# Performance work log

Measured on AMD Instinct MI355X. Metric: run time of the kernel, lower is better.

## Reference

```python
import jax, jax.numpy as jnp
import numpy as np

T, B, DIM, N = 2048, 16, 1024, 64
INIT_BETA_BIAS = 2.0
EPS = 1e-6


def setup_inputs() -> dict:
    key = jax.random.key(0)
    ks = jax.random.split(key, 6)
    xavier = np.sqrt(2.0 / (N + DIM)).astype(np.float32)
    return {
        "x": jax.random.normal(ks[0], (T, B, DIM), dtype=jnp.float32),
        "S0": jnp.zeros((B, N, N), dtype=jnp.float32),
        "W_k": jax.random.normal(ks[1], (N, DIM), dtype=jnp.float32) * xavier,
        "W_v": jax.random.normal(ks[2], (N, DIM), dtype=jnp.float32) * xavier,
        "W_q": jax.random.normal(ks[3], (N, DIM), dtype=jnp.float32) * xavier,
        "W_beta": jax.random.normal(ks[4], (N, DIM), dtype=jnp.float32) * xavier,
        "b_beta": jnp.full((N,), INIT_BETA_BIAS, dtype=jnp.float32),
    }


def reference(x, S0, W_k, W_v, W_q, W_beta, b_beta):
    # Batched projections: [T, B, dim] @ [dim, n] -> [T, B, n]
    k_all = jnp.einsum("tbd,nd->tbn", x, W_k)
    v_all = jnp.einsum("tbd,nd->tbn", x, W_v)
    q_all = jnp.einsum("tbd,nd->tbn", x, W_q)
    g_all = jax.nn.sigmoid(jnp.einsum("tbd,nd->tbn", x, W_beta) + b_beta)

    def step(S, inp):
        k, v, q, g = inp  # each [B, n]
        k_norm = k / (jnp.linalg.norm(k, axis=-1, keepdims=True) + EPS)
        retrieved = jnp.einsum("bij,bj->bi", S, k_norm)
        delta = v - retrieved
        S_new = g[:, :, None] * S + delta[:, :, None] * k_norm[:, None, :]
        Sq = jnp.einsum("bij,bj->bi", S_new, q)
        out = Sq * jax.nn.silu(Sq)  # self-gated output
        return S_new, out

    S_final, output = jax.lax.scan(step, S0, (k_all, v_all, q_all, g_all))
    return output, S_final
```

## Files before the change

kernel.cpp:

```cpp
#include <hip/hip_runtime.h>
#include <math.h>

#define T_STEPS 2048
#define BATCH   16
#define DIM     1024
#define NSTATE  64
#define NFIELD  256
#define PROJ_TSTRIDE (BATCH * NFIELD)
static constexpr float EPS = 1e-6f;

#define AS1 __attribute__((address_space(1)))
#define AS3 __attribute__((address_space(3)))

typedef _Float16 f16x8 __attribute__((ext_vector_type(8)));
typedef _Float16 f16x4 __attribute__((ext_vector_type(4)));
typedef float    f32x4 __attribute__((ext_vector_type(4)));

template <int CTRL>
__device__ __forceinline__ float dpp_pmul(float x) {
    int yi = __builtin_amdgcn_update_dpp(0x3f800000, __float_as_int(x),
                                         CTRL, 0xF, 0xF, false);
    return x * __int_as_float(yi);
}
template <int CTRL>
__device__ __forceinline__ float dpp_add(float x) {
    int yi = __builtin_amdgcn_update_dpp(0, __float_as_int(x), CTRL, 0xF, 0xF, true);
    return x + __int_as_float(yi);
}


#define PBM   128
#define KSTEP 64
#define NKS   (DIM / KSTEP)

__global__ __launch_bounds__(256) void prep_w16(
    const float* __restrict__ Wk, const float* __restrict__ Wv,
    const float* __restrict__ Wq, const float* __restrict__ Wb,
    _Float16* __restrict__ W16)
{
    const int flat = blockIdx.x * 256 + threadIdx.x;
    const int lane = flat & 63;
    const int st   = (flat >> 6) & 31;
    const int ks   = flat >> 11;
    const int cg = st & 15, kc2 = st >> 4;
    const int col = cg * 16 + (lane & 15);
    const int field = col >> 6, wrow = col & 63;
    const float* Wf = (field == 0 ? Wk : field == 1 ? Wv : field == 2 ? Wq : Wb);
    const float* src = Wf + (size_t)wrow * DIM + ks * 64 + kc2 * 32 + (lane >> 4) * 8;
    const float4 a = *(const float4*)(src);
    const float4 b = *(const float4*)(src + 4);
    f16x8 r;
    r[0] = (_Float16)a.x; r[1] = (_Float16)a.y; r[2] = (_Float16)a.z; r[3] = (_Float16)a.w;
    r[4] = (_Float16)b.x; r[5] = (_Float16)b.y; r[6] = (_Float16)b.z; r[7] = (_Float16)b.w;
    *(f16x8*)(W16 + (size_t)flat * 8) = r;
}

__global__ __launch_bounds__(512, 1) void proj_mfma(
    const float* __restrict__ x, const _Float16* __restrict__ W16,
    const float* __restrict__ bb, float* __restrict__ proj)
{
    __shared__ _Float16 Asub[2][16][64][8];
    __shared__ _Float16 Bsub[2][32][64][8];

    const int tid = threadIdx.x;
    const int w = tid >> 6, wl = tid & 63;
    const int wm = w >> 2, wn = w & 3;
    const int l15 = wl & 15, lr = wl >> 4;
    const size_t mbase = (size_t)blockIdx.x * PBM;

    _Float16* const abase = &Asub[0][0][0][0];
    _Float16* const bbase = &Bsub[0][0][0][0];

    const float* asrc[4];
    int aoff[4];
    #pragma unroll
    for (int it = 0; it < 4; ++it) {
        const int fid = it * 512 + tid;
        const int row = fid >> 4, kq = (fid & 15) * 4;
        asrc[it] = x + (mbase + row) * (size_t)DIM + kq;
        aoff[it] = ((kq >> 5) * 8 + (row >> 4)) * 512
                 + ((row & 15) + ((kq >> 3) & 3) * 16) * 8
                 + (kq & 7);
    }
    const _Float16* bsrc[4];
    int boff[4];
    #pragma unroll
    for (int m = 0; m < 4; ++m) {
        const int st = w * 4 + m;
        bsrc[m] = W16 + ((size_t)st * 64 + wl) * 8;
        boff[m] = st * 512;
    }

    auto stageB = [&](int ks, int buf) {
        #pragma unroll
        for (int m = 0; m < 4; ++m) {
            const _Float16* g = bsrc[m] + (size_t)ks * 16384;
            void* lp = (char*)bbase + (size_t)(buf * 16384 + boff[m]) * 2;
            __builtin_amdgcn_global_load_lds((const AS1 void*)g, (AS3 void*)lp, 16, 0, 0);
        }
    };

    float4 h0[4], h1[4];
    auto loadA = [&](int ks, float4* h) {
        #pragma unroll
        for (int it = 0; it < 4; ++it)
            h[it] = *(const float4*)(asrc[it] + ks * KSTEP);
    };
    auto writeA = [&](const float4* h, int buf) {
        #pragma unroll
        for (int it = 0; it < 4; ++it) {
            f16x4 v;
            v[0] = (_Float16)h[it].x; v[1] = (_Float16)h[it].y;
            v[2] = (_Float16)h[it].z; v[3] = (_Float16)h[it].w;
            *(f16x4*)(abase + buf * 8192 + aoff[it]) = v;
        }
    };

    f32x4 acc[4][4] = {};

    loadA(0, h0);
    stageB(0, 0);
    loadA(1, h1);
    writeA(h0, 0);
    __syncthreads();

    #pragma unroll
    for (int ks = 0; ks < NKS; ++ks) {
        const int buf = ks & 1;
        if (ks + 1 < NKS) stageB(ks + 1, buf ^ 1);
        if (ks + 2 < NKS) loadA(ks + 2, (ks & 1) ? h1 : h0);

        #pragma unroll
        for (int kc = 0; kc < 2; ++kc) {
            f16x8 af[4], bf[4];
            #pragma unroll
            for (int mf = 0; mf < 4; ++mf)
                af[mf] = *(const f16x8*)&Asub[buf][kc * 8 + wm * 4 + mf][wl][0];
            #pragma unroll
            for (int nf = 0; nf < 4; ++nf)
                bf[nf] = *(const f16x8*)&Bsub[buf][kc * 16 + wn * 4 + nf][wl][0];
            #pragma unroll
            for (int mf = 0; mf < 4; ++mf)
                #pragma unroll
                for (int nf = 0; nf < 4; ++nf)
                    acc[mf][nf] = __builtin_amdgcn_mfma_f32_16x16x32_f16(
                        af[mf], bf[nf], acc[mf][nf], 0, 0, 0);
        }

        if (ks + 1 < NKS) writeA((ks & 1) ? h0 : h1, buf ^ 1);
        __syncthreads();
    }

    if (wn == 0) {
        #pragma unroll
        for (int mf = 0; mf < 4; ++mf) {
            f32x4 s = acc[mf][0] * acc[mf][0];
            #pragma unroll
            for (int nf = 1; nf < 4; ++nf) s += acc[mf][nf] * acc[mf][nf];
            #pragma unroll
            for (int r = 0; r < 4; ++r) {
                float t = s[r];
                t += __shfl_xor(t, 1); t += __shfl_xor(t, 2);
                t += __shfl_xor(t, 4); t += __shfl_xor(t, 8);
                const float sc = 1.f / (sqrtf(t) + EPS);
                #pragma unroll
                for (int nf = 0; nf < 4; ++nf) acc[mf][nf][r] *= sc;
            }
        }
    }
    if (wn == 3) {
        #pragma unroll
        for (int nf = 0; nf < 4; ++nf) {
            const float bv = bb[nf * 16 + l15];
            #pragma unroll
            for (int mf = 0; mf < 4; ++mf)
                #pragma unroll
                for (int r = 0; r < 4; ++r)
                    acc[mf][nf][r] = 1.f / (1.f + __expf(-(acc[mf][nf][r] + bv)));
        }
    }

    #pragma unroll
    for (int mf = 0; mf < 4; ++mf)
        #pragma unroll
        for (int r = 0; r < 4; ++r) {
            float* dst = proj + (mbase + wm * 64 + mf * 16 + lr * 4 + r) * NFIELD
                              + wn * 64 + l15;
            dst[0]  = acc[mf][0][r];
            dst[16] = acc[mf][1][r];
            dst[32] = acc[mf][2][r];
            dst[48] = acc[mf][3][r];
        }
}


#define CH 32
#define NCHUNK (T_STEPS / CH)

__global__ __launch_bounds__(256) void mn_prep(
    const float* __restrict__ proj, float* __restrict__ MN)
{
    __shared__ float K[32][68], Q[32][68];
    const int bch = blockIdx.x;
    const int b = bch >> 6, ch = bch & 63;
    const int tid = threadIdx.x;

    {
        const int t0 = tid >> 3, pp = tid & 7;
        const float* base = proj + ((size_t)(ch * 32 + t0) * BATCH + b) * NFIELD;
        *(float4*)&K[t0][8 * pp]     = *(const float4*)(base + 8 * pp);
        *(float4*)&K[t0][8 * pp + 4] = *(const float4*)(base + 8 * pp + 4);
        *(float4*)&Q[t0][8 * pp]     = *(const float4*)(base + 128 + 8 * pp);
        *(float4*)&Q[t0][8 * pp + 4] = *(const float4*)(base + 128 + 8 * pp + 4);
    }
    __syncthreads();

    const int t = tid & 31, ub = tid >> 5;
    float mm[4] = {0.f, 0.f, 0.f, 0.f}, nn[4] = {0.f, 0.f, 0.f, 0.f};
    #pragma unroll 4
    for (int db = 0; db < 16; ++db) {
        const float4 kt = *(const float4*)&K[t][4 * db];
        #pragma unroll
        for (int uu = 0; uu < 4; ++uu) {
            const float4 ku = *(const float4*)&K[ub * 4 + uu][4 * db];
            const float4 qu = *(const float4*)&Q[ub * 4 + uu][4 * db];
            mm[uu] = fmaf(kt.x, ku.x, fmaf(kt.y, ku.y,
                     fmaf(kt.z, ku.z, fmaf(kt.w, ku.w, mm[uu]))));
            nn[uu] = fmaf(kt.x, qu.x, fmaf(kt.y, qu.y,
                     fmaf(kt.z, qu.z, fmaf(kt.w, qu.w, nn[uu]))));
        }
    }
    float* dstb = MN + ((size_t)bch * 32) * 64;
    #pragma unroll
    for (int uu = 0; uu < 4; ++uu) {
        const int u = ub * 4 + uu;
        dstb[(size_t)u * 64 + t]      = (t < u)  ? mm[uu] : 0.f;
        dstb[(size_t)u * 64 + 32 + t] = (t <= u) ? nn[uu] : 0.f;
    }
}


__global__ __launch_bounds__(256, 1) void scan_kernel(
    const float* __restrict__ proj,
    const float* __restrict__ MN,
    const float* __restrict__ S0,
    float* __restrict__ out,
    float* __restrict__ Sfin)
{
    __shared__ float KQ[2][CH][128];
    __shared__ float VGT[2][16][CH];
    __shared__ float SROW[8][64];

    const int tid  = threadIdx.x;
    const int w    = tid >> 6, wl = tid & 63;
    const int half = wl >> 5, u = wl & 31;
    const int gid  = 2 * w + half;
    const int b    = blockIdx.x >> 3;
    const int i0   = (blockIdx.x & 7) * 8;
    const int i    = i0 + gid;

    {
        const float2 s2 = *(const float2*)(S0 + ((size_t)(b * 64 + i)) * 64 + 2 * u);
        *(float2*)&SROW[gid][2 * u] = s2;
    }

    const float* pb = proj + (size_t)b * NFIELD;

    const int l31 = wl & 31;
    const int glq = wl & 15;
    const int hlf = (l31 >= 16);
    auto stage = [&](int c2, int nb) {
        const float* cbase = pb + (size_t)c2 * CH * PROJ_TSTRIDE;
        #pragma unroll
        for (int m = 0; m < 4; ++m) {
            const int n = w * 4 + m;
            const int s = 2 * n + (wl >> 5);
            const int field = (hlf ? 128 : 0) + 4 * (glq ^ (s & 7));
            const float* g = cbase + (size_t)s * PROJ_TSTRIDE + field;
            void* lp = (char*)&KQ[nb][0][0] + n * 1024;
            __builtin_amdgcn_global_load_lds((const AS1 void*)g, (AS3 void*)lp, 16, 0, 0);
        }
        #pragma unroll
        for (int m = 0; m < 2; ++m) {
            const int p = w * 2 + m;
            const int f = 2 * p + (wl >> 5);
            const int col = wl & 31;
            const int field = (f < 8) ? (64 + i0 + f) : (192 + i0 + (f - 8));
            const float* g = cbase + (size_t)col * PROJ_TSTRIDE + field;
            void* lp = (char*)&VGT[nb][0][0] + p * 256;
            __builtin_amdgcn_global_load_lds((const AS1 void*)g, (AS3 void*)lp, 4, 0, 0);
        }
    };

    stage(0, 0);
    __syncthreads();

    for (int c = 0; c < NCHUNK; ++c) {
        const int cb = c & 1;
        if (c + 1 < NCHUNK) stage(c + 1, cb ^ 1);

        const float (*KQc)[128] = KQ[cb];
        const float (*VGTc)[CH] = VGT[cb];

        float Mreg[32], Nreg[32];
        {
            const float* mnb = MN + (((size_t)b * NCHUNK + c) * 32 + u) * 64;
            #pragma unroll
            for (int k = 0; k < 8; ++k) {
                const float4 t4 = *(const float4*)(mnb + 4 * k);
                Mreg[4 * k] = t4.x; Mreg[4 * k + 1] = t4.y;
                Mreg[4 * k + 2] = t4.z; Mreg[4 * k + 3] = t4.w;
            }
            #pragma unroll
            for (int k = 0; k < 8; ++k) {
                const float4 t4 = *(const float4*)(mnb + 32 + 4 * k);
                Nreg[4 * k] = t4.x; Nreg[4 * k + 1] = t4.y;
                Nreg[4 * k + 2] = t4.z; Nreg[4 * k + 3] = t4.w;
            }
        }

        const float v_u = VGTc[gid][u];
        const float g_u = VGTc[8 + gid][u];
        float P = g_u;
        P = dpp_pmul<0x111>(P);
        P = dpp_pmul<0x112>(P);
        P = dpp_pmul<0x114>(P);
        P = dpp_pmul<0x118>(P);
        {
            const int t15 = __builtin_amdgcn_ds_swizzle(__float_as_int(P), (15 << 5));
            const float pl = __int_as_float(t15);
            P = (u >= 16) ? P * pl : P;
        }
        const float Pm1  = P / g_u;
        const float invP = 1.0f / P;

        float acc = 0.f, accq = 0.f;
        #pragma unroll
        for (int a4 = 0; a4 < 16; ++a4) {
            const int L = 4 * (a4 ^ (u & 7));
            const float4 s4 = *(const float4*)&SROW[gid][4 * a4];
            const float4 k4 = *(const float4*)&KQc[u][L];
            const float4 q4 = *(const float4*)&KQc[u][64 + L];
            acc  = fmaf(s4.x, k4.x, fmaf(s4.y, k4.y,
                   fmaf(s4.z, k4.z, fmaf(s4.w, k4.w, acc))));
            accq = fmaf(s4.x, q4.x, fmaf(s4.y, q4.y,
                   fmaf(s4.z, q4.z, fmaf(s4.w, q4.w, accq))));
        }

        float2 supd = make_float2(0.f, 0.f);
#define SWEEP_STEP(T)                                                          \
        {                                                                      \
            const float e_ = (v_u - Pm1 * acc) * invP;                         \
            const int ei_ = __builtin_amdgcn_ds_swizzle(__float_as_int(e_),    \
                                                        ((T) << 5));           \
            const float eb_ = __int_as_float(ei_);                             \
            acc  = fmaf(eb_, Mreg[T], acc);                                    \
            accq = fmaf(eb_, Nreg[T], accq);                                   \
            const float2 kk_ = *(const float2*)&KQc[T][(2 * u) ^ (4 * ((T) & 7))]; \
            supd.x = fmaf(eb_, kk_.x, supd.x);                                 \
            supd.y = fmaf(eb_, kk_.y, supd.y);                                 \
        }
        SWEEP_STEP(0)  SWEEP_STEP(1)  SWEEP_STEP(2)  SWEEP_STEP(3)
        SWEEP_STEP(4)  SWEEP_STEP(5)  SWEEP_STEP(6)  SWEEP_STEP(7)
        SWEEP_STEP(8)  SWEEP_STEP(9)  SWEEP_STEP(10) SWEEP_STEP(11)
        SWEEP_STEP(12) SWEEP_STEP(13) SWEEP_STEP(14) SWEEP_STEP(15)
        SWEEP_STEP(16) SWEEP_STEP(17) SWEEP_STEP(18) SWEEP_STEP(19)
        SWEEP_STEP(20) SWEEP_STEP(21) SWEEP_STEP(22) SWEEP_STEP(23)
        SWEEP_STEP(24) SWEEP_STEP(25) SWEEP_STEP(26) SWEEP_STEP(27)
        SWEEP_STEP(28) SWEEP_STEP(29) SWEEP_STEP(30) SWEEP_STEP(31)
#undef SWEEP_STEP

        {
            const int p31 = __builtin_amdgcn_ds_swizzle(__float_as_int(P), (31 << 5));
            const float Pc = __int_as_float(p31);
            float2 sold = *(const float2*)&SROW[gid][2 * u];
            sold.x = Pc * (sold.x + supd.x);
            sold.y = Pc * (sold.y + supd.y);
            *(float2*)&SROW[gid][2 * u] = sold;
        }
        {
            const float oq = P * accq;
            const float y = oq * oq / (1.f + __expf(-oq));
            out[((size_t)(c * CH + u) * BATCH + b) * 64 + i] = y;
        }

        __syncthreads();
    }

    {
        const float2 sf = *(const float2*)&SROW[gid][2 * u];
        *(float2*)(Sfin + ((size_t)(b * 64 + i)) * 64 + 2 * u) = sf;
    }
}

extern "C" void kernel_launch(void* const* d_in, const int* in_sizes, int n_in,
                              void* d_out, int out_size, void* d_ws, size_t ws_size,
                              hipStream_t stream) {
    const float* x  = (const float*)d_in[0];
    const float* S0 = (const float*)d_in[1];
    const float* Wk = (const float*)d_in[2];
    const float* Wv = (const float*)d_in[3];
    const float* Wq = (const float*)d_in[4];
    const float* Wb = (const float*)d_in[5];
    const float* bb = (const float*)d_in[6];

    float* out  = (float*)d_out;
    float* Sfin = out + (size_t)T_STEPS * BATCH * NSTATE;

    float*    proj = (float*)d_ws;
    float*    MN   = proj + (size_t)T_STEPS * BATCH * NFIELD;
    _Float16* W16  = (_Float16*)(MN + (size_t)BATCH * NCHUNK * 32 * 64);

    prep_w16<<<128, 256, 0, stream>>>(Wk, Wv, Wq, Wb, W16);
    proj_mfma<<<(T_STEPS * BATCH) / PBM, 512, 0, stream>>>(x, W16, bb, proj);
    mn_prep<<<BATCH * NCHUNK, 256, 0, stream>>>(proj, MN);
    scan_kernel<<<(BATCH * NSTATE) / 8, 256, 0, stream>>>(proj, MN, S0, out, Sfin);
}
```

Baseline: 422.0 us.

## Widen scan chunks to 64 steps with full-wave rows and fp16 MN staging

Chunk length doubles from 32 to 64 so each wave handles one state row across all 64 lanes. The per-chunk M/N correction matrices move to fp16 and are staged into LDS via async global-to-LDS loads instead of per-thread register loads. The sweep broadcasts through readlane instead of ds_swizzle, and outputs are staged in LDS for coalesced stores. The goal is to halve the number of chunk iterations and barriers and to raise parallelism, with 256 blocks instead of 128. The costs are a longer serial sweep per chunk, fp16 precision loss in the correction terms, and possible readlane overhead.

Result: faster. 385.6 us (-8.6%).

```diff
diff --git a/kernel.cpp b/kernel.cpp
--- a/kernel.cpp
+++ b/kernel.cpp
@@ -14,18 +14,17 @@
 
 typedef _Float16 f16x8 __attribute__((ext_vector_type(8)));
 typedef _Float16 f16x4 __attribute__((ext_vector_type(4)));
+typedef _Float16 f16x2 __attribute__((ext_vector_type(2)));
 typedef float    f32x4 __attribute__((ext_vector_type(4)));
 
-template <int CTRL>
+template <int CTRL, int RMASK>
 __device__ __forceinline__ float dpp_pmul(float x) {
     int yi = __builtin_amdgcn_update_dpp(0x3f800000, __float_as_int(x),
-                                         CTRL, 0xF, 0xF, false);
+                                         CTRL, RMASK, 0xF, false);
     return x * __int_as_float(yi);
 }
-template <int CTRL>
-__device__ __forceinline__ float dpp_add(float x) {
-    int yi = __builtin_amdgcn_update_dpp(0, __float_as_int(x), CTRL, 0xF, 0xF, true);
-    return x + __int_as_float(yi);
+__device__ __forceinline__ float rdlane(float x, int l) {
+    return __int_as_float(__builtin_amdgcn_readlane(__float_as_int(x), l));
 }
 
 
@@ -194,100 +193,122 @@
 }
 
 
-#define CH 32
+#define CH 64
 #define NCHUNK (T_STEPS / CH)
 
 __global__ __launch_bounds__(256) void mn_prep(
-    const float* __restrict__ proj, float* __restrict__ MN)
+    const float* __restrict__ proj, _Float16* __restrict__ MNg)
 {
-    __shared__ float K[32][68], Q[32][68];
+    __shared__ float K[64][68], Q[64][68];
     const int bch = blockIdx.x;
-    const int b = bch >> 6, ch = bch & 63;
+    const int bb2 = bch >> 5, ch = bch & 31;
     const int tid = threadIdx.x;
 
-    {
-        const int t0 = tid >> 3, pp = tid & 7;
-        const float* base = proj + ((size_t)(ch * 32 + t0) * BATCH + b) * NFIELD;
-        *(float4*)&K[t0][8 * pp]     = *(const float4*)(base + 8 * pp);
-        *(float4*)&K[t0][8 * pp + 4] = *(const float4*)(base + 8 * pp + 4);
-        *(float4*)&Q[t0][8 * pp]     = *(const float4*)(base + 128 + 8 * pp);
-        *(float4*)&Q[t0][8 * pp + 4] = *(const float4*)(base + 128 + 8 * pp + 4);
+    #pragma unroll
+    for (int it = 0; it < 8; ++it) {
+        const int s = it * 256 + tid;
+        const int row = s >> 5, half = (s >> 4) & 1, idx = s & 15;
+        const float* src = proj + ((size_t)(ch * 64 + row) * BATCH + bb2) * NFIELD
+                         + (half ? 128 : 0) + idx * 4;
+        const float4 v4 = *(const float4*)src;
+        if (half == 0) *(float4*)&K[row][idx * 4] = v4;
+        else           *(float4*)&Q[row][idx * 4] = v4;
     }
     __syncthreads();
 
-    const int t = tid & 31, ub = tid >> 5;
-    float mm[4] = {0.f, 0.f, 0.f, 0.f}, nn[4] = {0.f, 0.f, 0.f, 0.f};
-    #pragma unroll 4
-    for (int db = 0; db < 16; ++db) {
-        const float4 kt = *(const float4*)&K[t][4 * db];
-        #pragma unroll
-        for (int uu = 0; uu < 4; ++uu) {
-            const float4 ku = *(const float4*)&K[ub * 4 + uu][4 * db];
-            const float4 qu = *(const float4*)&Q[ub * 4 + uu][4 * db];
-            mm[uu] = fmaf(kt.x, ku.x, fmaf(kt.y, ku.y,
-                     fmaf(kt.z, ku.z, fmaf(kt.w, ku.w, mm[uu]))));
-            nn[uu] = fmaf(kt.x, qu.x, fmaf(kt.y, qu.y,
-                     fmaf(kt.z, qu.z, fmaf(kt.w, qu.w, nn[uu]))));
-        }
-    }
-    float* dstb = MN + ((size_t)bch * 32) * 64;
-    #pragma unroll
-    for (int uu = 0; uu < 4; ++uu) {
-        const int u = ub * 4 + uu;
-        dstb[(size_t)u * 64 + t]      = (t < u)  ? mm[uu] : 0.f;
-        dstb[(size_t)u * 64 + 32 + t] = (t <= u) ? nn[uu] : 0.f;
+    const int t0 = (tid >> 4) * 4, u0 = (tid & 15) * 4;
+    float m4[4][4] = {}, n4[4][4] = {};
+    #pragma unroll
+    for (int j4 = 0; j4 < 16; ++j4) {
+        float4 kt[4], ku[4], qu[4];
+        #pragma unroll
+        for (int r = 0; r < 4; ++r) {
+            kt[r] = *(const float4*)&K[t0 + r][4 * j4];
+            ku[r] = *(const float4*)&K[u0 + r][4 * j4];
+            qu[r] = *(const float4*)&Q[u0 + r][4 * j4];
+        }
+        #pragma unroll
+        for (int a2 = 0; a2 < 4; ++a2)
+            #pragma unroll
+            for (int c2 = 0; c2 < 4; ++c2) {
+                m4[a2][c2] = fmaf(kt[a2].x, ku[c2].x, fmaf(kt[a2].y, ku[c2].y,
+                             fmaf(kt[a2].z, ku[c2].z, fmaf(kt[a2].w, ku[c2].w, m4[a2][c2]))));
+                n4[a2][c2] = fmaf(kt[a2].x, qu[c2].x, fmaf(kt[a2].y, qu[c2].y,
+                             fmaf(kt[a2].z, qu[c2].z, fmaf(kt[a2].w, qu[c2].w, n4[a2][c2]))));
+            }
+    }
+    _Float16* dst = MNg + (size_t)bch * 64 * 128;
+    #pragma unroll
+    for (int a2 = 0; a2 < 4; ++a2) {
+        const int t = t0 + a2;
+        #pragma unroll
+        for (int c2 = 0; c2 < 4; ++c2) {
+            const int uu = u0 + c2;
+            f16x2 val;
+            val[0] = (_Float16)((uu > t)  ? m4[a2][c2] : 0.f);
+            val[1] = (_Float16)((uu >= t) ? n4[a2][c2] : 0.f);
+            *(f16x2*)&dst[(size_t)t * 128 + 2 * uu] = val;
+        }
     }
 }
 
 
 __global__ __launch_bounds__(256, 1) void scan_kernel(
     const float* __restrict__ proj,
-    const float* __restrict__ MN,
+    const _Float16* __restrict__ MNg,
     const float* __restrict__ S0,
     float* __restrict__ out,
     float* __restrict__ Sfin)
 {
-    __shared__ float KQ[2][CH][128];
-    __shared__ float VGT[2][16][CH];
-    __shared__ float SROW[8][64];
-
-    const int tid  = threadIdx.x;
-    const int w    = tid >> 6, wl = tid & 63;
-    const int half = wl >> 5, u = wl & 31;
-    const int gid  = 2 * w + half;
-    const int b    = blockIdx.x >> 3;
-    const int i0   = (blockIdx.x & 7) * 8;
-    const int i    = i0 + gid;
-
-    {
-        const float2 s2 = *(const float2*)(S0 + ((size_t)(b * 64 + i)) * 64 + 2 * u);
-        *(float2*)&SROW[gid][2 * u] = s2;
-    }
+    __shared__ float    KQ[2][CH][128];
+    __shared__ _Float16 MNh[2][CH][128];
+    __shared__ float    VG[2][CH][8];
+    __shared__ float    OUTb[2][CH][4];
+    __shared__ float    SROW[4][64];
+
+    const int tid = threadIdx.x;
+    const int w = tid >> 6, u = tid & 63;
+    const int b  = blockIdx.x >> 4;
+    const int i0 = (blockIdx.x & 15) * 4;
+    const int i  = i0 + w;
+
+    float S = S0[((size_t)(b * 64 + i)) * 64 + u];
+    SROW[w][u] = S;
 
     const float* pb = proj + (size_t)b * NFIELD;
-
-    const int l31 = wl & 31;
-    const int glq = wl & 15;
-    const int hlf = (l31 >= 16);
-    auto stage = [&](int c2, int nb) {
-        const float* cbase = pb + (size_t)c2 * CH * PROJ_TSTRIDE;
+    const _Float16* mnb = MNg + (size_t)b * NCHUNK * CH * 128;
+
+    const int kq_dw = (u & 31) * 4;
+    const int kq_f  = (kq_dw < 64) ? kq_dw : kq_dw + 64;
+    const int kq_t  = u >> 5;
+    const int mn_t  = u >> 4;
+    const int mn_by = (u & 15) * 16;
+    const int vg_t  = u >> 3;
+    const int vg_fi = u & 7;
+    const int vg_f  = (vg_fi < 4) ? (64 + i0 + vg_fi) : (192 + i0 + vg_fi - 4);
+
+    auto stage = [&](int c, int nb) {
+        const float* cbase = pb + (size_t)c * CH * PROJ_TSTRIDE;
+        #pragma unroll
+        for (int m = 0; m < 8; ++m) {
+            const int n = w * 8 + m;
+            const float* g = cbase + (size_t)(2 * n + kq_t) * PROJ_TSTRIDE + kq_f;
+            void* lp = (char*)&KQ[nb][0][0] + n * 1024;
+            __builtin_amdgcn_global_load_lds((const AS1 void*)g, (AS3 void*)lp, 16, 0, 0);
+        }
+        const char* mnc = (const char*)(mnb + (size_t)c * CH * 128);
         #pragma unroll
         for (int m = 0; m < 4; ++m) {
             const int n = w * 4 + m;
-            const int s = 2 * n + (wl >> 5);
-            const int field = (hlf ? 128 : 0) + 4 * (glq ^ (s & 7));
-            const float* g = cbase + (size_t)s * PROJ_TSTRIDE + field;
-            void* lp = (char*)&KQ[nb][0][0] + n * 1024;
+            const char* g = mnc + (size_t)(4 * n + mn_t) * 256 + mn_by;
+            void* lp = (char*)&MNh[nb][0][0] + n * 1024;
             __builtin_amdgcn_global_load_lds((const AS1 void*)g, (AS3 void*)lp, 16, 0, 0);
         }
         #pragma unroll
         for (int m = 0; m < 2; ++m) {
             const int p = w * 2 + m;
-            const int f = 2 * p + (wl >> 5);
-            const int col = wl & 31;
-            const int field = (f < 8) ? (64 + i0 + f) : (192 + i0 + (f - 8));
-            const float* g = cbase + (size_t)col * PROJ_TSTRIDE + field;
-            void* lp = (char*)&VGT[nb][0][0] + p * 256;
+            const float* g = cbase + (size_t)(p * 8 + vg_t) * PROJ_TSTRIDE + vg_f;
+            void* lp = (char*)&VG[nb][0][0] + p * 256;
             __builtin_amdgcn_global_load_lds((const AS1 void*)g, (AS3 void*)lp, 4, 0, 0);
         }
     };
@@ -296,101 +317,62 @@
     __syncthreads();
 
     for (int c = 0; c < NCHUNK; ++c) {
-        const int cb = c & 1;
-        if (c + 1 < NCHUNK) stage(c + 1, cb ^ 1);
-
-        const float (*KQc)[128] = KQ[cb];
-        const float (*VGTc)[CH] = VGT[cb];
-
-        float Mreg[32], Nreg[32];
-        {
-            const float* mnb = MN + (((size_t)b * NCHUNK + c) * 32 + u) * 64;
-            #pragma unroll
-            for (int k = 0; k < 8; ++k) {
-                const float4 t4 = *(const float4*)(mnb + 4 * k);
-                Mreg[4 * k] = t4.x; Mreg[4 * k + 1] = t4.y;
-                Mreg[4 * k + 2] = t4.z; Mreg[4 * k + 3] = t4.w;
-            }
-            #pragma unroll
-            for (int k = 0; k < 8; ++k) {
-                const float4 t4 = *(const float4*)(mnb + 32 + 4 * k);
-                Nreg[4 * k] = t4.x; Nreg[4 * k + 1] = t4.y;
-                Nreg[4 * k + 2] = t4.z; Nreg[4 * k + 3] = t4.w;
-            }
-        }
-
-        const float v_u = VGTc[gid][u];
-        const float g_u = VGTc[8 + gid][u];
+        const int cb2 = c & 1;
+        if (c + 1 < NCHUNK) stage(c + 1, cb2 ^ 1);
+
+        const float v_u = VG[cb2][u][w];
+        const float g_u = VG[cb2][u][4 + w];
         float P = g_u;
-        P = dpp_pmul<0x111>(P);
-        P = dpp_pmul<0x112>(P);
-        P = dpp_pmul<0x114>(P);
-        P = dpp_pmul<0x118>(P);
-        {
-            const int t15 = __builtin_amdgcn_ds_swizzle(__float_as_int(P), (15 << 5));
-            const float pl = __int_as_float(t15);
-            P = (u >= 16) ? P * pl : P;
-        }
-        const float Pm1  = P / g_u;
-        const float invP = 1.0f / P;
+        P = dpp_pmul<0x111, 0xF>(P);
+        P = dpp_pmul<0x112, 0xF>(P);
+        P = dpp_pmul<0x114, 0xF>(P);
+        P = dpp_pmul<0x118, 0xF>(P);
+        P = dpp_pmul<0x142, 0xA>(P);
+        P = dpp_pmul<0x143, 0xC>(P);
+        const float invP = __builtin_amdgcn_rcpf(P);
+        const float c1 = v_u * invP;
+        const float c2 = __builtin_amdgcn_rcpf(g_u);
 
         float acc = 0.f, accq = 0.f;
         #pragma unroll
-        for (int a4 = 0; a4 < 16; ++a4) {
-            const int L = 4 * (a4 ^ (u & 7));
-            const float4 s4 = *(const float4*)&SROW[gid][4 * a4];
-            const float4 k4 = *(const float4*)&KQc[u][L];
-            const float4 q4 = *(const float4*)&KQc[u][64 + L];
+        for (int j4 = 0; j4 < 16; ++j4) {
+            const int Cg = 4 * (j4 ^ (u & 15));
+            const float4 s4 = *(const float4*)&SROW[w][Cg];
+            const float4 k4 = *(const float4*)&KQ[cb2][u][Cg];
+            const float4 q4 = *(const float4*)&KQ[cb2][u][64 + Cg];
             acc  = fmaf(s4.x, k4.x, fmaf(s4.y, k4.y,
                    fmaf(s4.z, k4.z, fmaf(s4.w, k4.w, acc))));
             accq = fmaf(s4.x, q4.x, fmaf(s4.y, q4.y,
                    fmaf(s4.z, q4.z, fmaf(s4.w, q4.w, accq))));
         }
 
-        float2 supd = make_float2(0.f, 0.f);
-#define SWEEP_STEP(T)                                                          \
-        {                                                                      \
-            const float e_ = (v_u - Pm1 * acc) * invP;                         \
-            const int ei_ = __builtin_amdgcn_ds_swizzle(__float_as_int(e_),    \
-                                                        ((T) << 5));           \
-            const float eb_ = __int_as_float(ei_);                             \
-            acc  = fmaf(eb_, Mreg[T], acc);                                    \
-            accq = fmaf(eb_, Nreg[T], accq);                                   \
-            const float2 kk_ = *(const float2*)&KQc[T][(2 * u) ^ (4 * ((T) & 7))]; \
-            supd.x = fmaf(eb_, kk_.x, supd.x);                                 \
-            supd.y = fmaf(eb_, kk_.y, supd.y);                                 \
-        }
-        SWEEP_STEP(0)  SWEEP_STEP(1)  SWEEP_STEP(2)  SWEEP_STEP(3)
-        SWEEP_STEP(4)  SWEEP_STEP(5)  SWEEP_STEP(6)  SWEEP_STEP(7)
-        SWEEP_STEP(8)  SWEEP_STEP(9)  SWEEP_STEP(10) SWEEP_STEP(11)
-        SWEEP_STEP(12) SWEEP_STEP(13) SWEEP_STEP(14) SWEEP_STEP(15)
-        SWEEP_STEP(16) SWEEP_STEP(17) SWEEP_STEP(18) SWEEP_STEP(19)
-        SWEEP_STEP(20) SWEEP_STEP(21) SWEEP_STEP(22) SWEEP_STEP(23)
-        SWEEP_STEP(24) SWEEP_STEP(25) SWEEP_STEP(26) SWEEP_STEP(27)
-        SWEEP_STEP(28) SWEEP_STEP(29) SWEEP_STEP(30) SWEEP_STEP(31)
-#undef SWEEP_STEP
+        float supd = 0.f;
+        #pragma unroll
+        for (int T = 0; T < CH; ++T) {
+            const float e  = fmaf(-c2, acc, c1);
+            const float se = rdlane(e, T);
+            const f16x2 mn = *(const f16x2*)&MNh[cb2][T][2 * u];
+            const float kT = KQ[cb2][T][u];
+            acc  = fmaf(se, (float)mn[0], acc);
+            accq = fmaf(se, (float)mn[1], accq);
+            supd = fmaf(se, kT, supd);
+        }
+
+        const float Pc = rdlane(P, 63);
+        S = Pc * (S + supd);
+        SROW[w][u] = S;
+        const float oq = P * accq;
+        OUTb[cb2][u][w] = oq * oq / (1.f + __expf(-oq));
+
+        __syncthreads();
 
         {
-            const int p31 = __builtin_amdgcn_ds_swizzle(__float_as_int(P), (31 << 5));
-            const float Pc = __int_as_float(p31);
-            float2 sold = *(const float2*)&SROW[gid][2 * u];
-            sold.x = Pc * (sold.x + supd.x);
-            sold.y = Pc * (sold.y + supd.y);
-            *(float2*)&SROW[gid][2 * u] = sold;
-        }
-        {
-            const float oq = P * accq;
-            const float y = oq * oq / (1.f + __expf(-oq));
-            out[((size_t)(c * CH + u) * BATCH + b) * 64 + i] = y;
-        }
-
-        __syncthreads();
-    }
-
-    {
-        const float2 sf = *(const float2*)&SROW[gid][2 * u];
-        *(float2*)(Sfin + ((size_t)(b * 64 + i)) * 64 + 2 * u) = sf;
-    }
+            const int t = tid >> 2, col = tid & 3;
+            out[((size_t)(c * CH + t) * BATCH + b) * 64 + i0 + col] = OUTb[cb2][t][col];
+        }
+    }
+
+    Sfin[((size_t)(b * 64 + i)) * 64 + u] = S;
 }
 
 extern "C" void kernel_launch(void* const* d_in, const int* in_sizes, int n_in,
@@ -408,11 +390,11 @@
     float* Sfin = out + (size_t)T_STEPS * BATCH * NSTATE;
 
     float*    proj = (float*)d_ws;
-    float*    MN   = proj + (size_t)T_STEPS * BATCH * NFIELD;
-    _Float16* W16  = (_Float16*)(MN + (size_t)BATCH * NCHUNK * 32 * 64);
+    _Float16* MNg  = (_Float16*)(proj + (size_t)T_STEPS * BATCH * NFIELD);
+    _Float16* W16  = MNg + (size_t)BATCH * NCHUNK * CH * 128;
 
     prep_w16<<<128, 256, 0, stream>>>(Wk, Wv, Wq, Wb, W16);
     proj_mfma<<<(T_STEPS * BATCH) / PBM, 512, 0, stream>>>(x, W16, bb, proj);
-    mn_prep<<<BATCH * NCHUNK, 256, 0, stream>>>(proj, MN);
-    scan_kernel<<<(BATCH * NSTATE) / 8, 256, 0, stream>>>(proj, MN, S0, out, Sfin);
-}
+    mn_prep<<<BATCH * NCHUNK, 256, 0, stream>>>(proj, MNg);
+    scan_kernel<<<BATCH * 16, 256, 0, stream>>>(proj, MNg, S0, out, Sfin);
+}
```
